# Kernel optimization log

Hardware: AMD Instinct MI355X
Metric: run time of the kernel (lower is better)

## Reference

```python
import jax, jax.numpy as jnp
import numpy as np

POOL_SCALES = (1, 3, 6, 8)
CHANNELS = 256
BN_EPS = 1e-5


def _pool_matrix(in_size, out_size):
    # Row i averages input slots [floor(i*in/out), ceil((i+1)*in/out)) -- matches AdaptiveAvgPool2d.
    P = np.zeros((out_size, in_size), np.float32)
    for i in range(out_size):
        s = (i * in_size) // out_size
        e = -((-(i + 1) * in_size) // out_size)
        P[i, s:e] = 1.0 / (e - s)
    return jnp.asarray(P)


def _bn(x, g, b, m, v):
    # inference-mode BatchNorm2d on NCHW
    inv = g * jax.lax.rsqrt(v + BN_EPS)
    return x * inv[None, :, None, None] + (b - m * inv)[None, :, None, None]


def _conv1x1(x, w):
    # 1x1 conv == channel matmul: w [Cout, Cin], x [B, Cin, H, W]
    return jnp.einsum('oc,bchw->bohw', w, x)


def _ppm_concat(x):
    # x: [B, C, H, W] -> [B, C, sum(s*s)]
    B, C, H, W = x.shape
    outs = []
    for s in POOL_SCALES:
        Ph = _pool_matrix(H, s)
        Pw = _pool_matrix(W, s)
        pooled = jnp.einsum('ih,jw,bchw->bcij', Ph, Pw, x)
        outs.append(pooled.reshape(B, C, -1))
    return jnp.concatenate(outs, axis=2)


def setup_inputs() -> dict:
    key = jax.random.key(0)
    ks = jax.random.split(key, 24)
    B, Cl, Ch, Cmid, Cout, H, W = 8, 1024, 2048, 256, 2048, 64, 64
    return {
        'low_feats': jax.random.normal(ks[0], (B, Cl, H, W), jnp.float32),
        'high_feats': jax.random.normal(ks[1], (B, Ch, H, W), jnp.float32),
        'q_w': jax.random.normal(ks[2], (Cmid, Ch), jnp.float32) * 0.02,
        'q_g': jax.random.uniform(ks[3], (Cmid,), jnp.float32, 0.5, 1.5),
        'q_b': jax.random.normal(ks[4], (Cmid,), jnp.float32) * 0.1,
        'q_m': jax.random.normal(ks[5], (Cmid,), jnp.float32) * 0.1,
        'q_v': jax.random.uniform(ks[6], (Cmid,), jnp.float32, 0.5, 1.5),
        'k_w': jax.random.normal(ks[7], (Cmid, Cl), jnp.float32) * 0.02,
        'k_g': jax.random.uniform(ks[8], (Cmid,), jnp.float32, 0.5, 1.5),
        'k_b': jax.random.normal(ks[9], (Cmid,), jnp.float32) * 0.1,
        'k_m': jax.random.normal(ks[10], (Cmid,), jnp.float32) * 0.1,
        'k_v': jax.random.uniform(ks[11], (Cmid,), jnp.float32, 0.5, 1.5),
        'v_w': jax.random.normal(ks[12], (Cmid, Cl), jnp.float32) * 0.02,
        'v_b': jax.random.normal(ks[13], (Cmid,), jnp.float32) * 0.02,
        'o_w': jax.random.normal(ks[14], (Cout, Cmid), jnp.float32) * 0.02,
        'o_b': jax.random.normal(ks[15], (Cout,), jnp.float32) * 0.02,
        'bn_w': jax.random.normal(ks[16], (Cout, Cout + Ch), jnp.float32) * 0.02,
        'bn_g': jax.random.uniform(ks[17], (Cout,), jnp.float32, 0.5, 1.5),
        'bn_b': jax.random.normal(ks[18], (Cout,), jnp.float32) * 0.1,
        'bn_m': jax.random.normal(ks[19], (Cout,), jnp.float32) * 0.1,
        'bn_v': jax.random.uniform(ks[20], (Cout,), jnp.float32, 0.5, 1.5),
    }


def reference(low_feats, high_feats, q_w, q_g, q_b, q_m, q_v,
              k_w, k_g, k_b, k_m, k_v, v_w, v_b, o_w, o_b,
              bn_w, bn_g, bn_b, bn_m, bn_v):
    B, _, H, W = high_feats.shape
    # query: ConvModule (1x1 conv, BN, ReLU) on high-level feats; query_scale=1 -> no downsample
    q = jax.nn.relu(_bn(_conv1x1(high_feats, q_w), q_g, q_b, q_m, q_v))
    q = q.reshape(B, CHANNELS, H * W).transpose(0, 2, 1)  # [B, N, C]
    # key: ConvModule then pyramid-pooled; value: plain 1x1 conv then pyramid-pooled
    k = jax.nn.relu(_bn(_conv1x1(low_feats, k_w), k_g, k_b, k_m, k_v))
    k = _ppm_concat(k)  # [B, C, M]
    v = _conv1x1(low_feats, v_w) + v_b[None, :, None, None]
    v = _ppm_concat(v).transpose(0, 2, 1)  # [B, M, C]
    # matmul-normalized attention with pooled K/V (M = 110, tiny)
    sim = jnp.einsum('bnc,bcm->bnm', q, k) * (CHANNELS ** -0.5)
    sim = jax.nn.softmax(sim, axis=-1)
    ctx = jnp.einsum('bnm,bmc->bnc', sim, v)  # [B, N, C]
    ctx = ctx.transpose(0, 2, 1).reshape(B, CHANNELS, H, W)
    # out projection: plain 1x1 conv with bias
    ctx = _conv1x1(ctx, o_w) + o_b[None, :, None, None]  # [B, Cout, H, W]
    # single stage (query_scales=(1,)), stack+sum is identity
    # bottleneck: 1x1 conv (no bias) + BN, no activation
    fused = jnp.concatenate([ctx, high_feats], axis=1)
    out = _bn(_conv1x1(fused, bn_w), bn_g, bn_b, bn_m, bn_v)
    return out
```

## Files before the change

### kernel.cpp

```cpp
#include <hip/hip_runtime.h>
#include <hip/hip_bf16.h>

typedef unsigned int u32;
typedef unsigned short u16;
typedef short s16x8 __attribute__((ext_vector_type(8)));
typedef float f32x4 __attribute__((ext_vector_type(4)));
typedef u16 u16x4 __attribute__((ext_vector_type(4)));

__device__ __forceinline__ u16 f2b(float x) {
  u32 u = __float_as_uint(x);
  return (u16)((u + 0x7fffu + ((u >> 16) & 1u)) >> 16);
}
__device__ __forceinline__ float b2f(u16 x) { return __uint_as_float(((u32)x) << 16); }

__device__ __forceinline__ void gload16(const void* g, void* l) {
  __builtin_amdgcn_global_load_lds((const __attribute__((address_space(1))) u32*)g,
                                   (__attribute__((address_space(3))) u32*)l, 16, 0, 0);
}
__device__ __forceinline__ f32x4 mfma16(s16x8 a, s16x8 b, f32x4 c) {
  return __builtin_amdgcn_mfma_f32_16x16x32_bf16(a, b, c, 0, 0, 0);
}

template <int OUT_BF16>
__global__ __launch_bounds__(512, 2) void gemm256(
    const u16* __restrict__ A, long long sA, int lda,
    const u16* __restrict__ B1, long long sB1, int K1,
    const u16* __restrict__ B2, long long sB2, int K2,
    void* __restrict__ Cv, long long sC, int ldc,
    const float* __restrict__ bias, int bias_mode,
    int relu_limit, float alpha) {
  const int K = K1 + K2, nt = K >> 6;
  int tm, tn, b;
  {
    const int flat = blockIdx.x + gridDim.x * (blockIdx.y + gridDim.y * blockIdx.z);
    if (gridDim.z == 8) {
      const int slot = flat >> 3;
      b = flat & 7;
      tm = slot % gridDim.x;
      tn = slot / gridDim.x;
    } else { tm = blockIdx.x; tn = blockIdx.y; b = blockIdx.z; }
  }
  const u16* Ab = A + (size_t)b * sA + (size_t)tm * 256 * lda;
  const u16* B1b = B1 + (size_t)b * sB1 + (size_t)tn * 256 * K1;
  const u16* B2b = B2 ? (B2 + (size_t)b * sB2 + (size_t)tn * 256 * K2) : (const u16*)0;

  __shared__ __attribute__((aligned(128))) char lds[131072];

  const int tt = threadIdx.x, w = tt >> 6, l = tt & 63;
  const int wr = w >> 2, wc = w & 3;
  const int lr = l & 15, g16 = l >> 4;
  const int sxl = (lr & 7) << 4;

  auto stage_Aq = [&](int kt, int q) {
    const int bufB = (kt & 1) << 16;
    const int kk = kt << 6;
    const int lin = tt << 4;
    const int x = lin ^ (((lin >> 7) & 7) << 4);
    gload16(Ab + (size_t)((q << 6) + (x >> 7)) * lda + kk + ((x & 127) >> 1),
            lds + bufB + (q << 13) + (w << 10));
  };
  auto stage_Bh = [&](int kt, int h) {
    const int bufB = (kt & 1) << 16;
    const int kk = kt << 6;
    const u16* src; int ld, kcol;
    if (kk < K1) { src = B1b; ld = K1; kcol = kk; }
    else         { src = B2b; ld = K2; kcol = kk - K1; }
#pragma unroll
    for (int g = 0; g < 2; ++g) {
      const int lin = (g << 13) | (tt << 4);
      const int x = lin ^ (((lin >> 7) & 7) << 4);
      gload16(src + (size_t)((h << 7) + (x >> 7)) * ld + kcol + ((x & 127) >> 1),
              lds + bufB + 32768 + (h << 14) + (g << 13) + (w << 10));
    }
  };

  auto lda_frag = [&](const char* Al, int h, int kk, s16x8* af) {
#pragma unroll
    for (int i = 0; i < 4; ++i) {
      const int row = wr * 128 + (h * 4 + i) * 16 + lr;
      af[i] = *reinterpret_cast<const s16x8*>(
          Al + (row << 7) + (((kk << 6) | (g16 << 4)) ^ sxl));
    }
  };
  auto ldb_frag = [&](const char* Bl, int kk, s16x8* bf) {
#pragma unroll
    for (int n = 0; n < 4; ++n) {
      const int row = wc * 64 + n * 16 + lr;
      bf[n] = *reinterpret_cast<const s16x8*>(
          Bl + (row << 7) + (((kk << 6) | (g16 << 4)) ^ sxl));
    }
  };

  f32x4 acc[8][4] = {};

  auto mfma_q = [&](int h, const s16x8* af, const s16x8* bf) {
    __builtin_amdgcn_s_setprio(1);
#pragma unroll
    for (int i = 0; i < 4; ++i)
#pragma unroll
      for (int n = 0; n < 4; ++n)
        acc[h * 4 + i][n] = mfma16(af[i], bf[n], acc[h * 4 + i][n]);
    __builtin_amdgcn_s_setprio(0);
  };

  stage_Aq(0, 0); stage_Aq(0, 2); stage_Bh(0, 0); stage_Bh(0, 1);
  stage_Aq(0, 1); stage_Aq(0, 3);
  if (nt > 1) {
    stage_Aq(1, 0); stage_Aq(1, 2); stage_Bh(1, 0); stage_Bh(1, 1);
    asm volatile("s_waitcnt vmcnt(6)" ::: "memory");
  } else {
    asm volatile("s_waitcnt vmcnt(0)" ::: "memory");
  }
  __builtin_amdgcn_s_barrier();

  for (int t = 0; t < nt; ++t) {
    const char* Al = lds + ((t & 1) << 16);
    const char* Bl = Al + 32768;
    s16x8 bf0[4], bf1[4], af[4];

    lda_frag(Al, 0, 0, af);
    ldb_frag(Bl, 0, bf0);
    if (t + 1 < nt) { stage_Aq(t + 1, 1); stage_Aq(t + 1, 3); }
    __builtin_amdgcn_s_barrier();
    asm volatile("s_waitcnt lgkmcnt(0)" ::: "memory");
    mfma_q(0, af, bf0);
    __builtin_amdgcn_s_barrier();

    lda_frag(Al, 0, 1, af);
    ldb_frag(Bl, 1, bf1);
    __builtin_amdgcn_s_barrier();
    asm volatile("s_waitcnt lgkmcnt(0)" ::: "memory");
    mfma_q(0, af, bf1);
    __builtin_amdgcn_s_barrier();

    lda_frag(Al, 1, 0, af);
    if (t + 2 < nt) { stage_Aq(t + 2, 0); stage_Aq(t + 2, 2); stage_Bh(t + 2, 0); }
    __builtin_amdgcn_s_barrier();
    asm volatile("s_waitcnt lgkmcnt(0)" ::: "memory");
    mfma_q(1, af, bf0);
    __builtin_amdgcn_s_barrier();

    lda_frag(Al, 1, 1, af);
    if (t + 2 < nt) stage_Bh(t + 2, 1);
    __builtin_amdgcn_s_barrier();
    asm volatile("s_waitcnt lgkmcnt(0)" ::: "memory");
    mfma_q(1, af, bf1);
    if (t + 1 < nt) {
      if (t + 2 < nt) asm volatile("s_waitcnt vmcnt(6)" ::: "memory");
      else            asm volatile("s_waitcnt vmcnt(0)" ::: "memory");
    }
    __builtin_amdgcn_s_barrier();
  }

  const int li = g16 * 4;
#pragma unroll
  for (int m = 0; m < 8; ++m) {
    const int row = tm * 256 + wr * 128 + m * 16 + li;
#pragma unroll
    for (int j = 0; j < 4; ++j) {
      const int col = tn * 256 + wc * 64 + j * 16 + lr;
      const float bc = (bias_mode == 1) ? bias[col] : 0.f;
#pragma unroll
      for (int i = 0; i < 4; ++i) {
        float v = acc[m][j][i] * alpha;
        v += (bias_mode == 2) ? bias[row + i] : bc;
        if (col < relu_limit) v = fmaxf(v, 0.f);
        const size_t idx = (size_t)b * sC + (size_t)(row + i) * ldc + col;
        if (OUT_BF16) ((u16*)Cv)[idx] = f2b(v);
        else          ((float*)Cv)[idx] = v;
      }
    }
  }
}

template <int OUT_BF16>
__global__ __launch_bounds__(256) void gemm_bt(
    const u16* __restrict__ A, long long sA, int lda,
    const u16* __restrict__ B1, long long sB1, int K1,
    const u16* __restrict__ B2, long long sB2, int K2,
    void* __restrict__ Cv, long long sC, int ldc,
    const float* __restrict__ bias, int bias_mode,
    int relu_limit, float alpha) {
  const int K = K1 + K2;
  const int b = blockIdx.z;
  const int tm = blockIdx.x, tn = blockIdx.y;
  const u16* Ab = A + (size_t)b * sA;
  const u16* B1b = B1 + (size_t)b * sB1;
  const u16* B2b = B2 ? (B2 + (size_t)b * sB2) : (const u16*)0;

  __shared__ u16 As[128 * 32];
  __shared__ u16 Bs[128 * 32];

  const int t = threadIdx.x;
  const int w = t >> 6, l = t & 63;
  const int wr = w >> 1, wc = w & 1;
  const int srow = w * 16 + (l >> 2);
  const int scol = (l & 3) * 8;
  u16* AsW = As + w * 512;
  u16* BsW = Bs + w * 512;

  f32x4 acc[4][4] = {};
  const int lr = l & 15, lk = (l >> 4) * 8;

  for (int kk = 0; kk < K; kk += 32) {
    __syncthreads();
    {
      const u16* g0 = Ab + (size_t)(tm * 128 + srow) * lda + (kk + scol);
      gload16(g0, AsW);
      gload16(g0 + (size_t)64 * lda, AsW + 2048);
    }
    {
      const u16* bb; int ld, kloc;
      if (kk < K1) { bb = B1b; ld = K1; kloc = kk; }
      else         { bb = B2b; ld = K2; kloc = kk - K1; }
      const u16* g0 = bb + (size_t)(tn * 128 + srow) * ld + (kloc + scol);
      gload16(g0, BsW);
      gload16(g0 + (size_t)64 * ld, BsW + 2048);
    }
    __syncthreads();
    s16x8 af[4], bfr[4];
#pragma unroll
    for (int m = 0; m < 4; ++m)
      af[m] = *reinterpret_cast<const s16x8*>(&As[(wr * 64 + m * 16 + lr) * 32 + lk]);
#pragma unroll
    for (int j = 0; j < 4; ++j)
      bfr[j] = *reinterpret_cast<const s16x8*>(&Bs[(wc * 64 + j * 16 + lr) * 32 + lk]);
#pragma unroll
    for (int m = 0; m < 4; ++m)
#pragma unroll
      for (int j = 0; j < 4; ++j)
        acc[m][j] = mfma16(af[m], bfr[j], acc[m][j]);
  }

  const int li = (l >> 4) * 4;
#pragma unroll
  for (int m = 0; m < 4; ++m) {
    const int row = tm * 128 + wr * 64 + m * 16 + li;
#pragma unroll
    for (int j = 0; j < 4; ++j) {
      const int col = tn * 128 + wc * 64 + j * 16 + lr;
      const float bc = (bias_mode == 1) ? bias[col] : 0.f;
#pragma unroll
      for (int i = 0; i < 4; ++i) {
        float v = acc[m][j][i] * alpha;
        v += (bias_mode == 2) ? bias[row + i] : bc;
        if (col < relu_limit) v = fmaxf(v, 0.f);
        const size_t idx = (size_t)b * sC + (size_t)(row + i) * ldc + col;
        if (OUT_BF16) ((u16*)Cv)[idx] = f2b(v);
        else          ((float*)Cv)[idx] = v;
      }
    }
  }
}

__global__ __launch_bounds__(256) void transpose_cvt(
    const float* __restrict__ in, u16* __restrict__ out, int R, int C) {
  const int b = blockIdx.z;
  in += (size_t)b * R * C;
  out += (size_t)b * R * C;
  const int ct = blockIdx.x, rt = blockIdx.y;
  __shared__ float tile[64][65];
  const int t = threadIdx.x;
  {
    const int c4 = (t & 15) * 4, r0 = t >> 4;
    const float* src = in + (size_t)(rt * 64 + r0) * C + ct * 64 + c4;
#pragma unroll
    for (int i = 0; i < 4; ++i) {
      const float4 v = *reinterpret_cast<const float4*>(src + (size_t)(i * 16) * C);
      tile[r0 + i * 16][c4 + 0] = v.x; tile[r0 + i * 16][c4 + 1] = v.y;
      tile[r0 + i * 16][c4 + 2] = v.z; tile[r0 + i * 16][c4 + 3] = v.w;
    }
  }
  __syncthreads();
  {
    const int r4 = (t & 15) * 4, c0 = t >> 4;
    u16* dst = out + (size_t)(ct * 64 + c0) * R + rt * 64 + r4;
#pragma unroll
    for (int i = 0; i < 4; ++i) {
      u16x4 o;
      o.x = f2b(tile[r4 + 0][c0 + i * 16]);
      o.y = f2b(tile[r4 + 1][c0 + i * 16]);
      o.z = f2b(tile[r4 + 2][c0 + i * 16]);
      o.w = f2b(tile[r4 + 3][c0 + i * 16]);
      *reinterpret_cast<u16x4*>(dst + (size_t)(i * 16) * R) = o;
    }
  }
}

__global__ __launch_bounds__(256) void prep_wq(const float* __restrict__ qw,
    const float* __restrict__ qg, const float* __restrict__ qb_,
    const float* __restrict__ qm, const float* __restrict__ qv,
    u16* __restrict__ Wq, float* __restrict__ qbias) {
  const int i = blockIdx.x * 256 + threadIdx.x;
  const int o = i >> 11, c = i & 2047;
  const float inv = qg[o] * rsqrtf(qv[o] + 1e-5f);
  Wq[i] = f2b(qw[i] * inv);
  if (c == 0) qbias[o] = qb_[o] - qm[o] * inv;
}

__global__ __launch_bounds__(256) void prep_wkv(const float* __restrict__ kw,
    const float* __restrict__ kg, const float* __restrict__ kb,
    const float* __restrict__ km, const float* __restrict__ kv,
    const float* __restrict__ vw, const float* __restrict__ vb,
    u16* __restrict__ Wkv, float* __restrict__ kvbias) {
  const int i = blockIdx.x * 256 + threadIdx.x;
  const int r = i >> 10, c = i & 1023;
  if (r < 256) {
    const float inv = kg[r] * rsqrtf(kv[r] + 1e-5f);
    Wkv[i] = f2b(kw[i] * inv);
    if (c == 0) kvbias[r] = kb[r] - km[r] * inv;
  } else {
    Wkv[i] = f2b(vw[(size_t)(r - 256) * 1024 + c]);
    if (c == 0) kvbias[r] = vb[r - 256];
  }
}

__global__ __launch_bounds__(256) void prep_bn(const float* __restrict__ bn_w,
    const float* __restrict__ g, const float* __restrict__ v_,
    u16* __restrict__ bn1s, u16* __restrict__ Wfin) {
  const int i = blockIdx.x * 256 + threadIdx.x;
  const int o = i >> 11, j = i & 2047;
  const float inv = g[o] * rsqrtf(v_[o] + 1e-5f);
  bn1s[i] = f2b(bn_w[(size_t)o * 4096 + j] * inv);
  Wfin[(size_t)o * 2304 + j] = f2b(bn_w[(size_t)o * 4096 + 2048 + j] * inv);
}

__global__ __launch_bounds__(256) void prep_fbias(const float* __restrict__ bn_w,
    const float* __restrict__ o_b, const float* __restrict__ g,
    const float* __restrict__ bb, const float* __restrict__ m_,
    const float* __restrict__ v_, float* __restrict__ fbias) {
  const int o = blockIdx.x, t = threadIdx.x;
  float s = 0.f;
  for (int j = t; j < 2048; j += 256) s += bn_w[(size_t)o * 4096 + j] * o_b[j];
  for (int off = 32; off; off >>= 1) s += __shfl_xor(s, off);
  __shared__ float red[4];
  if ((t & 63) == 0) red[t >> 6] = s;
  __syncthreads();
  if (t == 0) {
    const float tot = red[0] + red[1] + red[2] + red[3];
    const float inv = g[o] * rsqrtf(v_[o] + 1e-5f);
    fbias[o] = inv * tot + bb[o] - m_[o] * inv;
  }
}

__device__ __forceinline__ void jj_to_range(int jj, int& s, int& j, int& c0, int& c1) {
  if (jj < 1)       { s = 1; j = jj; }
  else if (jj < 4)  { s = 3; j = jj - 1; }
  else if (jj < 10) { s = 6; j = jj - 4; }
  else              { s = 8; j = jj - 10; }
  c0 = (j * 64) / s;
  c1 = ((j + 1) * 64 + s - 1) / s;
}

__global__ __launch_bounds__(256) void pool_cols(const u16* __restrict__ kvT,
                                                 float* __restrict__ cp) {
  const int b = blockIdx.y, r = blockIdx.x, t = threadIdx.x;
  const u16* base = kvT + ((size_t)b * 4096 + (size_t)r * 64) * 512;
  const int ch0 = (t & 63) * 8;
  for (int jj = (t >> 6); jj < 18; jj += 4) {
    int s, j, c0, c1;
    jj_to_range(jj, s, j, c0, c1);
    float acc[8] = {0.f, 0.f, 0.f, 0.f, 0.f, 0.f, 0.f, 0.f};
    for (int c = c0; c < c1; ++c) {
      const s16x8 v = *reinterpret_cast<const s16x8*>(base + (size_t)c * 512 + ch0);
#pragma unroll
      for (int i = 0; i < 8; ++i) acc[i] += b2f((u16)v[i]);
    }
    float* o = cp + (((size_t)(b * 64 + r) * 18 + jj) * 512 + ch0);
    *reinterpret_cast<float4*>(o)     = make_float4(acc[0], acc[1], acc[2], acc[3]);
    *reinterpret_cast<float4*>(o + 4) = make_float4(acc[4], acc[5], acc[6], acc[7]);
  }
}

__global__ __launch_bounds__(256) void pool_rows(const float* __restrict__ cp,
    u16* __restrict__ Kp, u16* __restrict__ Vp) {
  const int b = blockIdx.y, m = blockIdx.x, t = threadIdx.x;
  if (m >= 110) {
    Kp[((size_t)b * 128 + m) * 256 + t] = 0;
    Vp[((size_t)b * 256 + t) * 128 + m] = 0;
    return;
  }
  int s, idx, jjbase;
  if (m < 1)       { s = 1; idx = m;      jjbase = 0; }
  else if (m < 10) { s = 3; idx = m - 1;  jjbase = 1; }
  else if (m < 46) { s = 6; idx = m - 10; jjbase = 4; }
  else             { s = 8; idx = m - 46; jjbase = 10; }
  const int i = idx / s, j = idx % s;
  const int jj = jjbase + j;
  const int r0 = (i * 64) / s, r1 = ((i + 1) * 64 + s - 1) / s;
  const int c0 = (j * 64) / s, c1 = ((j + 1) * 64 + s - 1) / s;
  float a0 = 0.f, a1 = 0.f;
  for (int r = r0; r < r1; ++r) {
    const float* px = cp + ((size_t)(b * 64 + r) * 18 + jj) * 512;
    a0 += px[t];
    a1 += px[t + 256];
  }
  const float inv = 1.f / (float)((r1 - r0) * (c1 - c0));
  Kp[((size_t)b * 128 + m) * 256 + t] = f2b(a0 * inv);
  Vp[((size_t)b * 256 + t) * 128 + m] = f2b(a1 * inv);
}

__global__ __launch_bounds__(256) void softmax_rows(const float* __restrict__ sim,
                                                    u16* __restrict__ P) {
  const int row = blockIdx.x * 4 + (threadIdx.x >> 6);
  const int l = threadIdx.x & 63;
  const float* s = sim + (size_t)row * 128;
  const float v0 = (l < 110) ? s[l] : -1e30f;
  const float v1 = (l + 64 < 110) ? s[l + 64] : -1e30f;
  float mx = fmaxf(v0, v1);
  for (int off = 32; off; off >>= 1) mx = fmaxf(mx, __shfl_xor(mx, off));
  const float e0 = (l < 110) ? __expf(v0 - mx) : 0.f;
  const float e1 = (l + 64 < 110) ? __expf(v1 - mx) : 0.f;
  float sum = e0 + e1;
  for (int off = 32; off; off >>= 1) sum += __shfl_xor(sum, off);
  const float inv = 1.f / sum;
  u16* p = P + (size_t)row * 128;
  p[l] = f2b(e0 * inv);
  p[l + 64] = f2b(e1 * inv);
}

extern "C" void kernel_launch(void* const* d_in, const int* in_sizes, int n_in,
                              void* d_out, int out_size, void* d_ws, size_t ws_size,
                              hipStream_t stream) {
  (void)in_sizes; (void)n_in; (void)out_size; (void)ws_size;
  const float* low  = (const float*)d_in[0];
  const float* high = (const float*)d_in[1];
  const float* q_w = (const float*)d_in[2];
  const float* q_g = (const float*)d_in[3];
  const float* q_b = (const float*)d_in[4];
  const float* q_m = (const float*)d_in[5];
  const float* q_v = (const float*)d_in[6];
  const float* k_w = (const float*)d_in[7];
  const float* k_g = (const float*)d_in[8];
  const float* k_b = (const float*)d_in[9];
  const float* k_m = (const float*)d_in[10];
  const float* k_v = (const float*)d_in[11];
  const float* v_w = (const float*)d_in[12];
  const float* v_b = (const float*)d_in[13];
  const float* o_w = (const float*)d_in[14];
  const float* o_b = (const float*)d_in[15];
  const float* bn_w = (const float*)d_in[16];
  const float* bn_g = (const float*)d_in[17];
  const float* bn_b = (const float*)d_in[18];
  const float* bn_m = (const float*)d_in[19];
  const float* bn_v = (const float*)d_in[20];
  float* out = (float*)d_out;

  char* ws = (char*)d_ws;
  size_t off = 0;
  auto alloc = [&](size_t bytes) -> char* {
    char* p = ws + off;
    off += (bytes + 255) & ~(size_t)255;
    return p;
  };
  u16* XhT  = (u16*)alloc(134217728ull);
  u16* qT   = (u16*)alloc(16777216ull);
  u16* XlT  = (u16*)alloc(67108864ull);
  u16* kvT  = (u16*)alloc(33554432ull);
  u16* ctxT = (u16*)alloc(16777216ull);
  u16* Kpool = (u16*)alloc(524288ull);
  u16* VpT   = (u16*)alloc(524288ull);
  u16* Wq   = (u16*)alloc(1048576ull);
  u16* Wkv  = (u16*)alloc(1048576ull);
  u16* Wfin = (u16*)alloc(9437184ull);
  float* qbias  = (float*)alloc(1024);
  float* kvbias = (float*)alloc(2048);
  float* fbias  = (float*)alloc(8192);
  u16* bn1s = qT;
  u16* owT  = ctxT;
  float* sim = (float*)XlT;
  float* cp  = (float*)((char*)XlT + 25165824ull);
  u16* P = kvT;

  prep_bn<<<16384, 256, 0, stream>>>(bn_w, bn_g, bn_v, bn1s, Wfin);
  prep_fbias<<<2048, 256, 0, stream>>>(bn_w, o_b, bn_g, bn_b, bn_m, bn_v, fbias);
  prep_wq<<<2048, 256, 0, stream>>>(q_w, q_g, q_b, q_m, q_v, Wq, qbias);
  prep_wkv<<<2048, 256, 0, stream>>>(k_w, k_g, k_b, k_m, k_v, v_w, v_b, Wkv, kvbias);
  transpose_cvt<<<dim3(4, 32, 1), 256, 0, stream>>>(o_w, owT, 2048, 256);
  gemm_bt<1><<<dim3(16, 2, 1), 256, 0, stream>>>(
      bn1s, 0, 2048, owT, 0, 2048, (const u16*)0, 0, 0,
      (void*)(Wfin + 2048), 0, 2304, (const float*)0, 0, 0, 1.0f);

  transpose_cvt<<<dim3(64, 32, 8), 256, 0, stream>>>(high, XhT, 2048, 4096);
  transpose_cvt<<<dim3(64, 16, 8), 256, 0, stream>>>(low, XlT, 1024, 4096);

  gemm_bt<1><<<dim3(32, 2, 8), 256, 0, stream>>>(
      XhT, 4096ll * 2048, 2048, Wq, 0, 2048, (const u16*)0, 0, 0,
      qT, 4096ll * 256, 256, qbias, 1, 256, 1.0f);
  gemm256<1><<<dim3(16, 2, 8), 512, 0, stream>>>(
      XlT, 4096ll * 1024, 1024, Wkv, 0, 1024, (const u16*)0, 0, 0,
      kvT, 4096ll * 512, 512, kvbias, 1, 256, 1.0f);
  pool_cols<<<dim3(64, 8), 256, 0, stream>>>(kvT, cp);
  pool_rows<<<dim3(128, 8), 256, 0, stream>>>(cp, Kpool, VpT);
  gemm_bt<0><<<dim3(32, 1, 8), 256, 0, stream>>>(
      qT, 4096ll * 256, 256, Kpool, 128ll * 256, 256, (const u16*)0, 0, 0,
      sim, 4096ll * 128, 128, (const float*)0, 0, 0, 0.0625f);
  softmax_rows<<<8192, 256, 0, stream>>>(sim, P);
  gemm_bt<1><<<dim3(32, 2, 8), 256, 0, stream>>>(
      P, 4096ll * 128, 128, VpT, 256ll * 128, 128, (const u16*)0, 0, 0,
      ctxT, 4096ll * 256, 256, (const float*)0, 0, 0, 1.0f);
  gemm256<0><<<dim3(8, 16, 8), 512, 0, stream>>>(
      Wfin, 0, 2304, XhT, 4096ll * 2048, 2048, ctxT, 4096ll * 256, 256,
      out, 2048ll * 4096, 4096, fbias, 2, 0, 1.0f);
}
```

Baseline: 767.0 us.

## Fuse QK^T, softmax and PV into a single attention kernel

Replaces the separate sim GEMM, row softmax and P·V GEMM with one kernel per 128-query block. K and V for the batch are staged into LDS with XOR swizzling, scores stay in registers, softmax is done with 16-lane shuffles, and probabilities go through LDS into the second MFMA. This removes the fp32 sim and bf16 P round trips through global memory plus two launches. In exchange it uses 128KB of LDS per block, which limits occupancy, and only 256 blocks are launched.

```diff
diff --git a/kernel.cpp b/kernel.cpp
--- a/kernel.cpp
+++ b/kernel.cpp
@@ -253,6 +253,109 @@
   }
 }
 
+__global__ __launch_bounds__(512) void attn_fused(
+    const u16* __restrict__ qT,
+    const u16* __restrict__ Kp,
+    const u16* __restrict__ Vp,
+    u16* __restrict__ ctxT) {
+  const int qb = blockIdx.x, b = blockIdx.y;
+  const int tt = threadIdx.x, w = tt >> 6, l = tt & 63;
+  const int lr = l & 15, hi = l >> 4;
+  __shared__ __attribute__((aligned(128))) char lds[131072];
+
+  const char* KpG = (const char*)(Kp + (size_t)b * 32768);
+  const char* VpG = (const char*)(Vp + (size_t)b * 32768);
+#pragma unroll
+  for (int g = 0; g < 8; ++g) {
+    const int lin = (g * 512 + tt) << 4;
+    gload16(KpG + (lin ^ (((lin >> 9) & 7) << 4)), lds + g * 8192 + w * 1024);
+  }
+#pragma unroll
+  for (int g = 0; g < 8; ++g) {
+    const int lin = (g * 512 + tt) << 4;
+    gload16(VpG + (lin ^ (((lin >> 8) & 7) << 4)), lds + 65536 + g * 8192 + w * 1024);
+  }
+
+  const u16* qG = qT + ((size_t)b * 4096 + qb * 128 + w * 16 + lr) * 256 + hi * 8;
+  s16x8 qf[8];
+#pragma unroll
+  for (int kk = 0; kk < 8; ++kk)
+    qf[kk] = *reinterpret_cast<const s16x8*>(qG + kk * 32);
+
+  asm volatile("s_waitcnt vmcnt(0)" ::: "memory");
+  __syncthreads();
+
+  f32x4 ps[8] = {};
+  for (int kk = 0; kk < 8; ++kk) {
+#pragma unroll
+    for (int j = 0; j < 8; ++j) {
+      const int y = (j * 16 + lr) * 512 + kk * 64 + hi * 16;
+      const s16x8 kf = *reinterpret_cast<const s16x8*>(lds + (y ^ (((y >> 9) & 7) << 4)));
+      ps[j] = mfma16(qf[kk], kf, ps[j]);
+    }
+  }
+  __syncthreads();
+
+#pragma unroll
+  for (int i = 0; i < 4; ++i) {
+    float m0 = -1e30f;
+#pragma unroll
+    for (int j = 0; j < 7; ++j) {
+      float v = ps[j][i] * 0.0625f;
+      if (j == 6 && lr >= 14) v = -1e30f;
+      m0 = fmaxf(m0, v);
+    }
+#pragma unroll
+    for (int off = 8; off; off >>= 1) m0 = fmaxf(m0, __shfl_xor(m0, off, 16));
+    float s0 = 0.f;
+#pragma unroll
+    for (int j = 0; j < 7; ++j) {
+      const float v = ps[j][i] * 0.0625f;
+      const float ev = (j == 6 && lr >= 14) ? 0.f : __expf(v - m0);
+      ps[j][i] = ev;
+      s0 += ev;
+    }
+    ps[7][i] = 0.f;
+#pragma unroll
+    for (int off = 8; off; off >>= 1) s0 += __shfl_xor(s0, off, 16);
+    const float inv = 1.f / s0;
+#pragma unroll
+    for (int j = 0; j < 8; ++j) ps[j][i] *= inv;
+  }
+
+  char* PL = lds + w * 4096;
+#pragma unroll
+  for (int j = 0; j < 8; ++j)
+#pragma unroll
+    for (int i = 0; i < 4; ++i) {
+      const int n = hi * 4 + i, m = j * 16 + lr;
+      const int y = n * 256 + m * 2;
+      *reinterpret_cast<u16*>(PL + (y ^ ((n & 7) << 4))) = f2b(ps[j][i]);
+    }
+  __syncthreads();
+
+  f32x4 pc[16] = {};
+  const char* VL = lds + 65536;
+#pragma unroll
+  for (int kk = 0; kk < 4; ++kk) {
+    const int ya = lr * 256 + kk * 64 + hi * 16;
+    const s16x8 pa = *reinterpret_cast<const s16x8*>(PL + (ya ^ ((lr & 7) << 4)));
+#pragma unroll
+    for (int jc = 0; jc < 16; ++jc) {
+      const int y = (jc * 16 + lr) * 256 + kk * 64 + hi * 16;
+      const s16x8 vf = *reinterpret_cast<const s16x8*>(VL + (y ^ (((y >> 8) & 7) << 4)));
+      pc[jc] = mfma16(pa, vf, pc[jc]);
+    }
+  }
+
+  u16* outp = ctxT + ((size_t)b * 4096 + qb * 128 + w * 16) * 256;
+#pragma unroll
+  for (int jc = 0; jc < 16; ++jc)
+#pragma unroll
+    for (int i = 0; i < 4; ++i)
+      outp[(size_t)(hi * 4 + i) * 256 + jc * 16 + lr] = f2b(pc[jc][i]);
+}
+
 __global__ __launch_bounds__(256) void transpose_cvt(
     const float* __restrict__ in, u16* __restrict__ out, int R, int C) {
   const int b = blockIdx.z;
@@ -398,25 +501,6 @@
   const float inv = 1.f / (float)((r1 - r0) * (c1 - c0));
   Kp[((size_t)b * 128 + m) * 256 + t] = f2b(a0 * inv);
   Vp[((size_t)b * 256 + t) * 128 + m] = f2b(a1 * inv);
-}
-
-__global__ __launch_bounds__(256) void softmax_rows(const float* __restrict__ sim,
-                                                    u16* __restrict__ P) {
-  const int row = blockIdx.x * 4 + (threadIdx.x >> 6);
-  const int l = threadIdx.x & 63;
-  const float* s = sim + (size_t)row * 128;
-  const float v0 = (l < 110) ? s[l] : -1e30f;
-  const float v1 = (l + 64 < 110) ? s[l + 64] : -1e30f;
-  float mx = fmaxf(v0, v1);
-  for (int off = 32; off; off >>= 1) mx = fmaxf(mx, __shfl_xor(mx, off));
-  const float e0 = (l < 110) ? __expf(v0 - mx) : 0.f;
-  const float e1 = (l + 64 < 110) ? __expf(v1 - mx) : 0.f;
-  float sum = e0 + e1;
-  for (int off = 32; off; off >>= 1) sum += __shfl_xor(sum, off);
-  const float inv = 1.f / sum;
-  u16* p = P + (size_t)row * 128;
-  p[l] = f2b(e0 * inv);
-  p[l + 64] = f2b(e1 * inv);
 }
 
 extern "C" void kernel_launch(void* const* d_in, const int* in_sizes, int n_in,
@@ -468,9 +552,7 @@
   float* fbias  = (float*)alloc(8192);
   u16* bn1s = qT;
   u16* owT  = ctxT;
-  float* sim = (float*)XlT;
   float* cp  = (float*)((char*)XlT + 25165824ull);
-  u16* P = kvT;
 
   prep_bn<<<16384, 256, 0, stream>>>(bn_w, bn_g, bn_v, bn1s, Wfin);
   prep_fbias<<<2048, 256, 0, stream>>>(bn_w, o_b, bn_g, bn_b, bn_m, bn_v, fbias);
@@ -492,13 +574,7 @@
       kvT, 4096ll * 512, 512, kvbias, 1, 256, 1.0f);
   pool_cols<<<dim3(64, 8), 256, 0, stream>>>(kvT, cp);
   pool_rows<<<dim3(128, 8), 256, 0, stream>>>(cp, Kpool, VpT);
-  gemm_bt<0><<<dim3(32, 1, 8), 256, 0, stream>>>(
-      qT, 4096ll * 256, 256, Kpool, 128ll * 256, 256, (const u16*)0, 0, 0,
-      sim, 4096ll * 128, 128, (const float*)0, 0, 0, 0.0625f);
-  softmax_rows<<<8192, 256, 0, stream>>>(sim, P);
-  gemm_bt<1><<<dim3(32, 2, 8), 256, 0, stream>>>(
-      P, 4096ll * 128, 128, VpT, 256ll * 128, 128, (const u16*)0, 0, 0,
-      ctxT, 4096ll * 256, 256, (const float*)0, 0, 0, 1.0f);
+  attn_fused<<<dim3(32, 8), 512, 0, stream>>>(qT, Kpool, VpT, ctxT);
   gemm256<0><<<dim3(8, 16, 8), 512, 0, stream>>>(
       Wfin, 0, 2304, XhT, 4096ll * 2048, 2048, ctxT, 4096ll * 256, 256,
       out, 2048ll * 4096, 4096, fbias, 2, 0, 1.0f);
```

Measured after the change: 736.8 us. 3.9% less time.
